# Optimization experiments

Measured on AMD Instinct MI355X. Metric: run time of the kernel, lower is better.

## Reference

```python
import jax, jax.numpy as jnp
import numpy as np

T, S, B, D, H, F, E = 1024, 1024, 4, 1024, 16, 4096, 8
HD = D // H
N = T * B                      # tokens entering MoE
CAP = 2 * N // E               # top-2 capacity per expert


def setup_inputs() -> dict:
    key = jax.random.key(0)
    ks = jax.random.split(key, 16)
    sc = 0.02
    rn = lambda k, shp, s=sc: jax.random.normal(k, shp, jnp.float32) * s
    return {
        "tgt": jax.random.normal(ks[0], (T, B, D), jnp.float32),
        "memory": jax.random.normal(ks[1], (S, B, D), jnp.float32),
        "sa_in_w": rn(ks[2], (3 * D, D)), "sa_in_b": jnp.zeros((3 * D,), jnp.float32),
        "sa_out_w": rn(ks[3], (D, D)), "sa_out_b": jnp.zeros((D,), jnp.float32),
        "ca_in_w": rn(ks[4], (3 * D, D)), "ca_in_b": jnp.zeros((3 * D,), jnp.float32),
        "ca_out_w": rn(ks[5], (D, D)), "ca_out_b": jnp.zeros((D,), jnp.float32),
        "ln1_g": jnp.ones((D,), jnp.float32), "ln1_b": jnp.zeros((D,), jnp.float32),
        "ln2_g": jnp.ones((D,), jnp.float32), "ln2_b": jnp.zeros((D,), jnp.float32),
        "ln3_g": jnp.ones((D,), jnp.float32), "ln3_b": jnp.zeros((D,), jnp.float32),
        "wg": rn(ks[6], (D, E)),
        "w1": rn(ks[7], (E, D, F)), "b1": jnp.zeros((E, F), jnp.float32),
        "w2": rn(ks[8], (E, F, D)), "b2": jnp.zeros((E, D), jnp.float32),
    }


def layer_norm(x, g, b, eps=1e-5):
    mu = jnp.mean(x, axis=-1, keepdims=True)
    var = jnp.var(x, axis=-1, keepdims=True)
    return (x - mu) * jax.lax.rsqrt(var + eps) * g + b


def mha(q_in, k_in, v_in, in_w, in_b, out_w, out_b):
    # q_in: [Tq,B,D], k_in/v_in: [Tk,B,D]; torch MultiheadAttention math (eval)
    wq, wk, wv = jnp.split(in_w, 3, axis=0)
    bq, bk, bv = jnp.split(in_b, 3)
    def heads(x, w, bias):
        y = x @ w.T + bias                       # [Tx,B,D]
        return y.reshape(x.shape[0], B, H, HD).transpose(1, 2, 0, 3)  # [B,H,Tx,hd]
    q, k, v = heads(q_in, wq, bq), heads(k_in, wk, bk), heads(v_in, wv, bv)
    scores = jnp.einsum('bhtd,bhsd->bhts', q, k) / np.sqrt(HD)
    attn = jax.nn.softmax(scores, axis=-1)
    o = jnp.einsum('bhts,bhsd->bhtd', attn, v)   # [B,H,Tq,hd]
    o = o.transpose(2, 0, 1, 3).reshape(q_in.shape[0], B, D)
    return o @ out_w.T + out_b


def moe_top2(x, wg, w1, b1, w2, b2):
    # x: [N,D]. Top-2 gating with capacity dispatch + grouped expert FFN.
    logits = x @ wg                               # [N,E]
    gates = jax.nn.softmax(logits, axis=-1)
    idx1 = jnp.argmax(gates, axis=-1)             # [N]
    m1 = jax.nn.one_hot(idx1, E, dtype=x.dtype)   # [N,E]
    gates_wo1 = jnp.where(m1 > 0, -jnp.inf, logits)
    idx2 = jnp.argmax(gates_wo1, axis=-1)
    m2 = jax.nn.one_hot(idx2, E, dtype=x.dtype)
    ar = jnp.arange(N)
    g1 = gates[ar, idx1]
    g2 = gates[ar, idx2]
    denom = g1 + g2 + 1e-9
    g1, g2 = g1 / denom, g2 / denom
    # positions within each expert buffer (first-come-first-serve, top1 before top2)
    pos1 = jnp.cumsum(m1, axis=0)[ar, idx1] - 1
    counts1 = jnp.sum(m1, axis=0)                 # [E]
    pos2 = jnp.cumsum(m2, axis=0)[ar, idx2] - 1 + counts1[idx2]
    keep1 = (pos1 < CAP).astype(x.dtype)
    keep2 = (pos2 < CAP).astype(x.dtype)
    p1 = jnp.clip(pos1, 0, CAP - 1).astype(jnp.int32)
    p2 = jnp.clip(pos2, 0, CAP - 1).astype(jnp.int32)
    buf = jnp.zeros((E, CAP, D), x.dtype)
    buf = buf.at[idx1, p1].add(x * keep1[:, None])
    buf = buf.at[idx2, p2].add(x * keep2[:, None])
    # grouped expert FFN: [E,CAP,D] -> [E,CAP,F] -> [E,CAP,D]
    h = jax.nn.relu(jnp.einsum('ecd,edf->ecf', buf, w1) + b1[:, None, :])
    eo = jnp.einsum('ecf,efd->ecd', h, w2) + b2[:, None, :]
    out = eo[idx1, p1] * (g1 * keep1)[:, None] + eo[idx2, p2] * (g2 * keep2)[:, None]
    return out


def reference(tgt, memory, sa_in_w, sa_in_b, sa_out_w, sa_out_b,
              ca_in_w, ca_in_b, ca_out_w, ca_out_b,
              ln1_g, ln1_b, ln2_g, ln2_b, ln3_g, ln3_b,
              wg, w1, b1, w2, b2):
    t2 = mha(tgt, tgt, tgt, sa_in_w, sa_in_b, sa_out_w, sa_out_b)
    x = layer_norm(tgt + t2, ln1_g, ln1_b)
    t2 = mha(x, memory, memory, ca_in_w, ca_in_b, ca_out_w, ca_out_b)
    x = layer_norm(x + t2, ln2_g, ln2_b)
    m = moe_top2(x.reshape(N, D), wg, w1, b1, w2, b2).reshape(T, B, D)
    x = layer_norm(x + m, ln3_g, ln3_b)
    return x
```

## Files before the change

kernel.cpp:

```cpp
#include <hip/hip_runtime.h>
#include <hip/hip_bf16.h>


typedef __bf16 bf16;
typedef __bf16 bf16x2 __attribute__((ext_vector_type(2)));
typedef __bf16 bf16x4 __attribute__((ext_vector_type(4)));
typedef __bf16 bf16x8 __attribute__((ext_vector_type(8)));
typedef float  f32x4  __attribute__((ext_vector_type(4)));

static_assert(sizeof(bf16) == 2, "bf16 size");

#define CAP_ 1024

#define GLOAD16(g, l)                                                  \
  __builtin_amdgcn_global_load_lds(                                    \
      (const __attribute__((address_space(1))) unsigned int*)(g),      \
      (__attribute__((address_space(3))) unsigned int*)(l), 16, 0, 0)

#define BAR() do { asm volatile("" ::: "memory"); __builtin_amdgcn_s_barrier(); asm volatile("" ::: "memory"); } while (0)

static const long OFF_WSAIN  = 0L;
static const long OFF_WSAOUT = 6291456L;
static const long OFF_WCAIN  = 8388608L;
static const long OFF_WCAOUT = 14680064L;
static const long OFF_BTGT   = 16777216L;
static const long OFF_BMEM   = 25165824L;
static const long OFF_QKV    = 33554432L;
static const long OFF_EO1    = 33554432L;
static const long OFF_KVCA   = OFF_QKV + 8388608L;
static const long OFF_VT     = 58720256L;
static const long OFF_AO     = 67108864L;
static const long OFF_PROJ   = 75497472L;
static const long OFF_X1     = 92274688L;
static const long OFF_X2     = 109051904L;
static const long OFF_SCORES = 125829120L;
static const long OFF_H      = OFF_SCORES + 67108864L;
static const long OFF_GATE   = 260046848L;
static const long OFF_E1   = OFF_GATE;
static const long OFF_E2   = OFF_GATE + 16384L;
static const long OFF_G1   = OFF_GATE + 32768L;
static const long OFF_G2   = OFF_GATE + 49152L;
static const long OFF_D1   = OFF_GATE + 65536L;
static const long OFF_D2   = OFF_GATE + 81920L;
static const long OFF_S1   = OFF_GATE + 98304L;
static const long OFF_S2   = OFF_GATE + 114688L;

__device__ __forceinline__ int xcd_swz(int bid, int nwg) {
  int q = nwg >> 3, r = nwg & 7;
  int xcd = bid & 7, idx = bid >> 3;
  return (xcd < r ? xcd * (q + 1) : r * (q + 1) + (xcd - r) * q) + idx;
}

__global__ __launch_bounds__(256) void k_cvt6(
    const float* __restrict__ s0, const float* __restrict__ s1,
    const float* __restrict__ s2, const float* __restrict__ s3,
    const float* __restrict__ s4, const float* __restrict__ s5,
    bf16* __restrict__ d0, bf16* __restrict__ d1, bf16* __restrict__ d2,
    bf16* __restrict__ d3, bf16* __restrict__ d4, bf16* __restrict__ d5) {
  long b = blockIdx.x;
  const float* s; bf16* d; long off;
  if (b < 3072)       { s = s0; d = d0; off = b; }
  else if (b < 4096)  { s = s1; d = d1; off = b - 3072; }
  else if (b < 7168)  { s = s2; d = d2; off = b - 4096; }
  else if (b < 8192)  { s = s3; d = d3; off = b - 7168; }
  else if (b < 12288) { s = s4; d = d4; off = b - 8192; }
  else                { s = s5; d = d5; off = b - 12288; }
  long i = off * 256 + threadIdx.x;
  float4 v = ((const float4*)s)[i];
  bf16x4 o = {(bf16)v.x, (bf16)v.y, (bf16)v.z, (bf16)v.w};
  ((bf16x4*)d)[i] = o;
}

__global__ __launch_bounds__(256) void k_transpose_f32_bf16(const float* __restrict__ in,
                                                            bf16* __restrict__ out, int R, int C) {
  __shared__ float t[64][70];
  int z = blockIdx.z;
  long r0 = (long)blockIdx.y * 64, c0 = (long)blockIdx.x * 64;
  const float* ib = in + (long)z * R * C;
  bf16* ob = out + (long)z * R * C;
  int x = threadIdx.x, y = threadIdx.y;
  #pragma unroll
  for (int j = 0; j < 4; j++) {
    int sr = y + j * 16;
    float4 v = *(const float4*)&ib[(r0 + sr) * C + c0 + x * 4];
    t[sr][x * 4 + 0] = v.x; t[sr][x * 4 + 1] = v.y;
    t[sr][x * 4 + 2] = v.z; t[sr][x * 4 + 3] = v.w;
  }
  __syncthreads();
  #pragma unroll
  for (int j = 0; j < 4; j++) {
    int sc = y + j * 16;
    #pragma unroll
    for (int i = 0; i < 2; i++) {
      int sr = x * 2 + i * 32;
      bf16x2 o = {(bf16)t[sr][sc], (bf16)t[sr + 1][sc]};
      *(bf16x2*)&ob[(c0 + sc) * R + r0 + sr] = o;
    }
  }
}

__global__ __launch_bounds__(256) void k_extract_vt(const bf16* __restrict__ in,
                                                    bf16* __restrict__ out, long rs, long sb) {
  __shared__ bf16 t[64][66];
  int z = blockIdx.z;
  long r0 = (long)blockIdx.y * 64;
  const bf16* ib = in + (long)(z >> 4) * sb + (long)(z & 15) * 64;
  bf16* ob = out + (long)z * 64 * 1024;
  int x = threadIdx.x, y = threadIdx.y;
  #pragma unroll
  for (int i = y; i < 64; i += 4) t[i][x] = ib[(r0 + i) * rs + x];
  __syncthreads();
  #pragma unroll
  for (int i = y; i < 64; i += 4) ob[(long)i * 1024 + r0 + x] = t[x][i];
}

template <int BM, int BN, int WM, int WN, bool RELU, typename OutT>
__global__ __launch_bounds__(256) void k_gemm_nt(
    const bf16* __restrict__ A, const bf16* __restrict__ Bp,
    OutT* __restrict__ C, const float* __restrict__ bias,
    int K, long lda, long ldb, long ldc, float alpha, int zdiv,
    long sA1, long sA0, long sB1, long sB0, long sC1, long sC0,
    long sBias1, long sBias0) {
  constexpr int BK = 32;
  constexpr int WTM = BM / WM, WTN = BN / WN, MR = WTM / 16, NR = WTN / 16;
  constexpr int AISS = BM * BK / 2048;
  constexpr int BISS = BN * BK / 2048;
  __shared__ bf16 sa[BM * BK];
  __shared__ bf16 sb[BN * BK];
  const int nwg = gridDim.x * gridDim.y * gridDim.z;
  const int bid = blockIdx.x + gridDim.x * (blockIdx.y + gridDim.y * blockIdx.z);
  const int lid = xcd_swz(bid, nwg);
  const int bx = lid % gridDim.x;
  const int rem = lid / gridDim.x;
  const int by = rem % gridDim.y;
  const int z = rem / gridDim.y;
  const int zh = z / zdiv, zl = z - zh * zdiv;
  const bf16* Ab = A + zh * sA1 + zl * sA0 + (long)by * BM * lda;
  const bf16* Bb = Bp + zh * sB1 + zl * sB0 + (long)bx * BN * ldb;
  const int tid = threadIdx.x, lane = tid & 63, wid = tid >> 6;
  const int wm = wid / WN, wn = wid % WN;

  const int srow = tid >> 2;
  const int scol = (tid & 3) * 8;
  const bf16* aptr[AISS];
  bf16* aldst[AISS];
  #pragma unroll
  for (int i = 0; i < AISS; i++) {
    aptr[i] = Ab + (long)(srow + i * 64) * lda + scol;
    aldst[i] = &sa[i * 2048 + (wid << 9)];
  }
  const bf16* bptr[BISS];
  bf16* bldst[BISS];
  #pragma unroll
  for (int i = 0; i < BISS; i++) {
    bptr[i] = Bb + (long)(srow + i * 64) * ldb + scol;
    bldst[i] = &sb[i * 2048 + (wid << 9)];
  }

  f32x4 acc[MR][NR] = {};
  const int rA = wm * WTM + (lane & 15);
  const int rB = wn * WTN + (lane & 15);
  const int kk = (lane >> 4) * 8;

  for (int k0 = 0; k0 < K; k0 += BK) {
    #pragma unroll
    for (int i = 0; i < AISS; i++) GLOAD16(aptr[i] + k0, aldst[i]);
    #pragma unroll
    for (int i = 0; i < BISS; i++) GLOAD16(bptr[i] + k0, bldst[i]);
    __syncthreads();
    bf16x8 af[MR], bfr[NR];
    #pragma unroll
    for (int mi = 0; mi < MR; mi++) af[mi] = *(const bf16x8*)&sa[(rA + mi * 16) * BK + kk];
    #pragma unroll
    for (int ni = 0; ni < NR; ni++) bfr[ni] = *(const bf16x8*)&sb[(rB + ni * 16) * BK + kk];
    #pragma unroll
    for (int mi = 0; mi < MR; mi++)
      #pragma unroll
      for (int ni = 0; ni < NR; ni++)
        acc[mi][ni] = __builtin_amdgcn_mfma_f32_16x16x32_bf16(af[mi], bfr[ni], acc[mi][ni], 0, 0, 0);
    __syncthreads();
  }
  OutT* Cb = C + zh * sC1 + zl * sC0;
  const float* biasb = bias ? (bias + zh * sBias1 + zl * sBias0) : nullptr;
  const long rowBase = (long)by * BM + wm * WTM + ((lane >> 4) * 4);
  const long colBase = (long)bx * BN + wn * WTN + (lane & 15);
  #pragma unroll
  for (int mi = 0; mi < MR; mi++) {
    #pragma unroll
    for (int ni = 0; ni < NR; ni++) {
      long col = colBase + ni * 16;
      float bv = biasb ? biasb[col] : 0.f;
      #pragma unroll
      for (int r = 0; r < 4; r++) {
        long row = rowBase + mi * 16 + r;
        float v = acc[mi][ni][r] * alpha + bv;
        if (RELU) v = fmaxf(v, 0.f);
        Cb[row * ldc + col] = (OutT)v;
      }
    }
  }
}

template <bool RELU, typename OutT>
__global__ __launch_bounds__(512, 2) void k_gemm8p(
    const bf16* __restrict__ A, const bf16* __restrict__ Bp,
    OutT* __restrict__ C, const float* __restrict__ bias,
    int K, long lda, long ldb, long ldc, int zdiv,
    long sA1, long sA0, long sB1, long sB0, long sC1, long sC0, long sBias1) {
  __shared__ bf16 smem[65536];
  const int nwg = gridDim.x * gridDim.y * gridDim.z;
  const int bid = blockIdx.x + gridDim.x * (blockIdx.y + gridDim.y * blockIdx.z);
  const int lid = xcd_swz(bid, nwg);
  const int bx = lid % gridDim.x;
  const int rem = lid / gridDim.x;
  const int by = rem % gridDim.y;
  const int z = rem / gridDim.y;
  const int zh = z / zdiv, zl = z - zh * zdiv;
  const bf16* Ab = A + zh * sA1 + zl * sA0 + (long)by * 256 * lda;
  const bf16* Bb = Bp + zh * sB1 + zl * sB0 + (long)bx * 256 * ldb;
  const int tid = threadIdx.x, lane = tid & 63, wid = tid >> 6;
  const int wm = wid >> 2, wn = wid & 3;
  const int lane15 = lane & 15, grp = lane >> 4;
  const int s_r = (wid << 3) + (lane >> 3);
  const int s_k = ((lane & 7) ^ (lane >> 3)) << 3;
  const int ldst = wid << 9;
  const int in0 = (grp << 4) ^ ((lane & 7) << 4);
  const int in1 = (64 | (grp << 4)) ^ ((lane & 7) << 4);

  const int NT = K >> 6;
  f32x4 acc[8][4] = {};
  bf16x8 a[4][2], b[2][2][2];

  const bf16* pA[4];
  const bf16* pB[4];
  #pragma unroll
  for (int q = 0; q < 4; q++) {
    pA[q] = Ab + (long)((q << 6) + s_r) * lda + s_k;
    pB[q] = Bb + (long)((q << 6) + s_r) * ldb + s_k;
  }

  auto loadA = [&](int mh, int cb) {
    #pragma unroll
    for (int mi2 = 0; mi2 < 4; mi2++) {
      int r = wm * 128 + mh * 64 + mi2 * 16 + lane15;
      a[mi2][0] = *(const bf16x8*)&smem[cb + (r << 6) + (in0 >> 1)];
      a[mi2][1] = *(const bf16x8*)&smem[cb + (r << 6) + (in1 >> 1)];
    }
  };
  auto loadB = [&](int nh, int cb) {
    #pragma unroll
    for (int ni2 = 0; ni2 < 2; ni2++) {
      int c = wn * 64 + nh * 32 + ni2 * 16 + lane15;
      b[nh][ni2][0] = *(const bf16x8*)&smem[cb + 16384 + (c << 6) + (in0 >> 1)];
      b[nh][ni2][1] = *(const bf16x8*)&smem[cb + 16384 + (c << 6) + (in1 >> 1)];
    }
  };
  auto mfmaQ = [&](int mh, int nh) {
    __builtin_amdgcn_s_setprio(1);
    #pragma unroll
    for (int ks = 0; ks < 2; ks++)
      #pragma unroll
      for (int mi2 = 0; mi2 < 4; mi2++)
        #pragma unroll
        for (int ni2 = 0; ni2 < 2; ni2++)
          acc[mh * 4 + mi2][nh * 2 + ni2] = __builtin_amdgcn_mfma_f32_16x16x32_bf16(
              a[mi2][ks], b[nh][ni2][ks], acc[mh * 4 + mi2][nh * 2 + ni2], 0, 0, 0);
    __builtin_amdgcn_s_setprio(0);
  };

  #pragma unroll
  for (int q = 0; q < 4; q++) {
    GLOAD16(pA[q], &smem[(q << 12) + ldst]);
    GLOAD16(pB[q], &smem[16384 + (q << 12) + ldst]);
  }
  #pragma unroll
  for (int q = 0; q < 4; q++) {
    GLOAD16(pA[q] + 64, &smem[32768 + (q << 12) + ldst]);
    GLOAD16(pB[q] + 64, &smem[32768 + 16384 + (q << 12) + ldst]);
  }
  asm volatile("s_waitcnt vmcnt(8)" ::: "memory");
  BAR();

  for (int t = 0; t < NT; t++) {
    const int cb = (t & 1) << 15;
    const bool dostage = (t + 2) < NT;
    loadA(0, cb); loadB(0, cb);
    BAR(); mfmaQ(0, 0); BAR();
    loadB(1, cb);
    if (dostage) {
      GLOAD16(pA[0] + 128, &smem[cb + ldst]);
      GLOAD16(pA[2] + 128, &smem[cb + (2 << 12) + ldst]);
    }
    BAR(); mfmaQ(0, 1); BAR();
    loadA(1, cb);
    if (dostage) {
      GLOAD16(pB[0] + 128, &smem[cb + 16384 + ldst]);
      GLOAD16(pB[1] + 128, &smem[cb + 16384 + (1 << 12) + ldst]);
    }
    BAR(); mfmaQ(1, 1); BAR();
    if (dostage) {
      GLOAD16(pA[1] + 128, &smem[cb + (1 << 12) + ldst]);
      GLOAD16(pA[3] + 128, &smem[cb + (3 << 12) + ldst]);
      GLOAD16(pB[2] + 128, &smem[cb + 16384 + (2 << 12) + ldst]);
      GLOAD16(pB[3] + 128, &smem[cb + 16384 + (3 << 12) + ldst]);
      asm volatile("s_waitcnt vmcnt(8)" ::: "memory");
    } else if (t + 1 < NT) {
      asm volatile("s_waitcnt vmcnt(0)" ::: "memory");
    }
    BAR(); mfmaQ(1, 0); BAR();
    #pragma unroll
    for (int q = 0; q < 4; q++) { pA[q] += 64; pB[q] += 64; }
  }

  OutT* Cb = C + zh * sC1 + zl * sC0;
  const float* biasb = bias ? (bias + zh * sBias1) : nullptr;
  float bv[4];
  #pragma unroll
  for (int ni = 0; ni < 4; ni++)
    bv[ni] = biasb ? biasb[(long)bx * 256 + wn * 64 + ni * 16 + lane15] : 0.f;
  const long rowBase = (long)by * 256 + wm * 128 + grp * 4;
  const long colBase = (long)bx * 256 + wn * 64 + lane15;
  #pragma unroll
  for (int mi = 0; mi < 8; mi++) {
    #pragma unroll
    for (int ni = 0; ni < 4; ni++) {
      long col = colBase + ni * 16;
      #pragma unroll
      for (int r = 0; r < 4; r++) {
        long row = rowBase + mi * 16 + r;
        float v = acc[mi][ni][r] + bv[ni];
        if (RELU) v = fmaxf(v, 0.f);
        Cb[row * ldc + col] = (OutT)v;
      }
    }
  }
}

__global__ __launch_bounds__(256) void k_flash(
    const bf16* __restrict__ q, const bf16* __restrict__ kk,
    const bf16* __restrict__ vt, bf16* __restrict__ ao,
    long qrs, long krs) {
  __shared__ bf16 kt[2][2048];
  __shared__ bf16 vtt[2][2048];
  __shared__ bf16 p_lds[4][32 * 72];
  const int nwg = gridDim.x * gridDim.y;
  const int bid = blockIdx.x + gridDim.x * blockIdx.y;
  const int lid = xcd_swz(bid, nwg);
  const int qt = lid & 7;
  const int bh = lid >> 3;
  const int b = bh >> 4, h = bh & 15;
  const int tid = threadIdx.x, lane = tid & 63, wid = tid >> 6;
  const int colLane = lane & 15, grp = lane >> 4;
  const bf16* qb = q + (qrs >> 2) * b + h * 64;
  const bf16* kb = kk + (krs >> 2) * b + h * 64;
  const bf16* vb = vt + (long)bh * 65536;

  bf16x8 qf[2][2];
  const int qrow0 = qt * 128 + wid * 32 + colLane;
  #pragma unroll
  for (int mi = 0; mi < 2; mi++)
    #pragma unroll
    for (int ks = 0; ks < 2; ks++)
      qf[mi][ks] = *(const bf16x8*)&qb[(long)(qrow0 + mi * 16) * qrs + ks * 32 + grp * 8];

  const int srow = tid >> 2;
  const int scol = (tid & 3) * 8;

  f32x4 oacc[2][4] = {};
  float m_[2][4], l_[2][4];
  #pragma unroll
  for (int mi = 0; mi < 2; mi++)
    #pragma unroll
    for (int r = 0; r < 4; r++) { m_[mi][r] = -INFINITY; l_[mi][r] = 0.f; }
  bf16* pl = &p_lds[wid][0];

  for (int s0 = 0; s0 < 1024; s0 += 64) {
    GLOAD16(&kb[(long)(s0 + srow) * krs + scol], &kt[0][wid << 9]);
    GLOAD16(&kb[(long)(s0 + srow) * krs + 32 + scol], &kt[1][wid << 9]);
    GLOAD16(&vb[(long)srow * 1024 + s0 + scol], &vtt[0][wid << 9]);
    GLOAD16(&vb[(long)srow * 1024 + s0 + 32 + scol], &vtt[1][wid << 9]);
    __syncthreads();

    f32x4 sacc[2][4] = {};
    bf16x8 kf[4][2];
    #pragma unroll
    for (int ni = 0; ni < 4; ni++)
      #pragma unroll
      for (int ks = 0; ks < 2; ks++)
        kf[ni][ks] = *(const bf16x8*)&kt[ks][(colLane + ni * 16) * 32 + grp * 8];
    #pragma unroll
    for (int ks = 0; ks < 2; ks++)
      #pragma unroll
      for (int mi = 0; mi < 2; mi++)
        #pragma unroll
        for (int ni = 0; ni < 4; ni++)
          sacc[mi][ni] = __builtin_amdgcn_mfma_f32_16x16x32_bf16(qf[mi][ks], kf[ni][ks], sacc[mi][ni], 0, 0, 0);

    float mnew[2][4], sc[2][4], psum[2][4];
    #pragma unroll
    for (int mi = 0; mi < 2; mi++)
      #pragma unroll
      for (int r = 0; r < 4; r++) {
        float vx = fmaxf(fmaxf(sacc[mi][0][r], sacc[mi][1][r]),
                         fmaxf(sacc[mi][2][r], sacc[mi][3][r])) * 0.125f;
        #pragma unroll
        for (int o = 1; o < 16; o <<= 1) vx = fmaxf(vx, __shfl_xor(vx, o));
        float mn = fmaxf(m_[mi][r], vx);
        sc[mi][r] = __expf(m_[mi][r] - mn);
        m_[mi][r] = mn; mnew[mi][r] = mn;
        l_[mi][r] *= sc[mi][r];
        psum[mi][r] = 0.f;
      }
    #pragma unroll
    for (int mi = 0; mi < 2; mi++)
      #pragma unroll
      for (int ni = 0; ni < 4; ni++)
        #pragma unroll
        for (int r = 0; r < 4; r++)
          oacc[mi][ni][r] *= sc[mi][r];
    #pragma unroll
    for (int mi = 0; mi < 2; mi++)
      #pragma unroll
      for (int ni = 0; ni < 4; ni++)
        #pragma unroll
        for (int r = 0; r < 4; r++) {
          float p = __expf(sacc[mi][ni][r] * 0.125f - mnew[mi][r]);
          psum[mi][r] += p;
          pl[(mi * 16 + grp * 4 + r) * 72 + ni * 16 + colLane] = (bf16)p;
        }
    #pragma unroll
    for (int mi = 0; mi < 2; mi++)
      #pragma unroll
      for (int r = 0; r < 4; r++) {
        float ps = psum[mi][r];
        #pragma unroll
        for (int o = 1; o < 16; o <<= 1) ps += __shfl_xor(ps, o);
        l_[mi][r] += ps;
      }

    bf16x8 pa[2][2], vf[4][2];
    #pragma unroll
    for (int mi = 0; mi < 2; mi++)
      #pragma unroll
      for (int ks = 0; ks < 2; ks++)
        pa[mi][ks] = *(const bf16x8*)&pl[(colLane + mi * 16) * 72 + ks * 32 + grp * 8];
    #pragma unroll
    for (int ni = 0; ni < 4; ni++)
      #pragma unroll
      for (int ks = 0; ks < 2; ks++)
        vf[ni][ks] = *(const bf16x8*)&vtt[ks][(colLane + ni * 16) * 32 + grp * 8];
    #pragma unroll
    for (int ks = 0; ks < 2; ks++)
      #pragma unroll
      for (int mi = 0; mi < 2; mi++)
        #pragma unroll
        for (int ni = 0; ni < 4; ni++)
          oacc[mi][ni] = __builtin_amdgcn_mfma_f32_16x16x32_bf16(pa[mi][ks], vf[ni][ks], oacc[mi][ni], 0, 0, 0);
    __syncthreads();
  }

  #pragma unroll
  for (int mi = 0; mi < 2; mi++)
    #pragma unroll
    for (int r = 0; r < 4; r++) {
      float inv = 1.f / l_[mi][r];
      int t = qt * 128 + wid * 32 + mi * 16 + grp * 4 + r;
      long n = (long)t * 4 + b;
      #pragma unroll
      for (int ni = 0; ni < 4; ni++)
        ao[n * 1024 + h * 64 + ni * 16 + colLane] = (bf16)(oacc[mi][ni][r] * inv);
    }
}

__global__ __launch_bounds__(256) void k_add_ln(const float* __restrict__ a, const float* __restrict__ b,
                                                const float* __restrict__ g, const float* __restrict__ be,
                                                float* __restrict__ out, bf16* __restrict__ outb) {
  long row = blockIdx.x;
  int tid = threadIdx.x;
  const float* pa = a + row * 1024;
  const float* pb = b + row * 1024;
  float v[4];
  float s = 0.f, sq = 0.f;
  #pragma unroll
  for (int i = 0; i < 4; i++) {
    int c = tid + i * 256;
    float x = pa[c] + pb[c];
    v[i] = x; s += x; sq += x * x;
  }
  #pragma unroll
  for (int o = 32; o; o >>= 1) { s += __shfl_xor(s, o); sq += __shfl_xor(sq, o); }
  __shared__ float r1[4], r2[4];
  int wid = tid >> 6;
  if ((tid & 63) == 0) { r1[wid] = s; r2[wid] = sq; }
  __syncthreads();
  s = r1[0] + r1[1] + r1[2] + r1[3];
  sq = r2[0] + r2[1] + r2[2] + r2[3];
  float mu = s * (1.f / 1024.f);
  float var = sq * (1.f / 1024.f) - mu * mu;
  float rstd = rsqrtf(var + 1e-5f);
  #pragma unroll
  for (int i = 0; i < 4; i++) {
    int c = tid + i * 256;
    float y = (v[i] - mu) * rstd * g[c] + be[c];
    out[row * 1024 + c] = y;
    if (outb) outb[row * 1024 + c] = (bf16)y;
  }
}

__global__ __launch_bounds__(256) void k_gate(const float* __restrict__ x, const float* __restrict__ wg,
                                              int* __restrict__ e1, int* __restrict__ e2,
                                              float* __restrict__ g1, float* __restrict__ g2) {
  int n = blockIdx.x * 4 + (threadIdx.x >> 6);
  int lane = threadIdx.x & 63;
  const float* xr = x + (long)n * 1024;
  float acc[8] = {0.f, 0.f, 0.f, 0.f, 0.f, 0.f, 0.f, 0.f};
  for (int i = 0; i < 16; i++) {
    float xv = xr[i * 64 + lane];
    const float* wr = wg + (long)(i * 64 + lane) * 8;
    #pragma unroll
    for (int e = 0; e < 8; e++) acc[e] += xv * wr[e];
  }
  #pragma unroll
  for (int e = 0; e < 8; e++)
    #pragma unroll
    for (int o = 32; o; o >>= 1) acc[e] += __shfl_xor(acc[e], o);
  if (lane == 0) {
    int i1 = 0; float b1v = acc[0];
    #pragma unroll
    for (int e = 1; e < 8; e++) if (acc[e] > b1v) { b1v = acc[e]; i1 = e; }
    int i2 = -1; float b2v = -INFINITY;
    #pragma unroll
    for (int e = 0; e < 8; e++) if (e != i1 && acc[e] > b2v) { b2v = acc[e]; i2 = e; }
    float den = 0.f;
    #pragma unroll
    for (int e = 0; e < 8; e++) den += __expf(acc[e] - b1v);
    float gg1 = 1.f / den;
    float gg2 = __expf(b2v - b1v) / den;
    float dn = gg1 + gg2 + 1e-9f;
    e1[n] = i1; e2[n] = i2; g1[n] = gg1 / dn; g2[n] = gg2 / dn;
  }
}

__global__ __launch_bounds__(256) void k_positions(const int* __restrict__ e1, const int* __restrict__ e2,
                                                   const float* __restrict__ g1, const float* __restrict__ g2,
                                                   int* __restrict__ d1, int* __restrict__ d2,
                                                   float* __restrict__ s1, float* __restrict__ s2) {
  const int e = blockIdx.x;
  const int tid = threadIdx.x, lane = tid & 63, wid = tid >> 6;
  __shared__ int wsum[4];
  int f[16];
  int cnt = 0;
  #pragma unroll
  for (int i = 0; i < 16; i++) { f[i] = (e1[tid * 16 + i] == e) ? 1 : 0; cnt += f[i]; }
  int inc = cnt;
  #pragma unroll
  for (int o = 1; o < 64; o <<= 1) { int v = __shfl_up(inc, o); if (lane >= o) inc += v; }
  if (lane == 63) wsum[wid] = inc;
  __syncthreads();
  int base = inc - cnt;
  for (int w = 0; w < wid; w++) base += wsum[w];
  const int total1 = wsum[0] + wsum[1] + wsum[2] + wsum[3];
  int run = base;
  #pragma unroll
  for (int i = 0; i < 16; i++) {
    int n = tid * 16 + i;
    if (f[i]) {
      int p = run++;
      d1[n] = e * CAP_ + (p < CAP_ ? p : CAP_ - 1);
      s1[n] = (p < CAP_) ? g1[n] : 0.f;
    }
  }
  cnt = 0;
  #pragma unroll
  for (int i = 0; i < 16; i++) { f[i] = (e2[tid * 16 + i] == e) ? 1 : 0; cnt += f[i]; }
  inc = cnt;
  #pragma unroll
  for (int o = 1; o < 64; o <<= 1) { int v = __shfl_up(inc, o); if (lane >= o) inc += v; }
  __syncthreads();
  if (lane == 63) wsum[wid] = inc;
  __syncthreads();
  base = inc - cnt + total1;
  for (int w = 0; w < wid; w++) base += wsum[w];
  run = base;
  #pragma unroll
  for (int i = 0; i < 16; i++) {
    int n = tid * 16 + i;
    if (f[i]) {
      int p = run++;
      d2[n] = e * CAP_ + (p < CAP_ ? p : CAP_ - 1);
      s2[n] = (p < CAP_) ? g2[n] : 0.f;
    }
  }
}

__global__ __launch_bounds__(256) void k_scatter(const float* __restrict__ x, const int* __restrict__ d1,
                                                 const int* __restrict__ d2, const float* __restrict__ s1,
                                                 const float* __restrict__ s2, bf16* __restrict__ buf) {
  int n = blockIdx.x;
  int tid = threadIdx.x;
  const float* xr = x + (long)n * 1024;
  float v[4];
  #pragma unroll
  for (int i = 0; i < 4; i++) v[i] = xr[tid + i * 256];
  if (s1[n] != 0.f) {
    bf16* o = buf + (long)d1[n] * 1024;
    #pragma unroll
    for (int i = 0; i < 4; i++) o[tid + i * 256] = (bf16)v[i];
  }
  if (s2[n] != 0.f) {
    bf16* o = buf + (long)d2[n] * 1024;
    #pragma unroll
    for (int i = 0; i < 4; i++) o[tid + i * 256] = (bf16)v[i];
  }
}

__global__ __launch_bounds__(256) void k_gather_ln(const float* __restrict__ x,
                                                   const bf16* __restrict__ p0, const bf16* __restrict__ p1,
                                                   const float* __restrict__ b2,
                                                   const int* __restrict__ d1, const int* __restrict__ d2,
                                                   const float* __restrict__ s1, const float* __restrict__ s2,
                                                   const float* __restrict__ g, const float* __restrict__ be,
                                                   float* __restrict__ out) {
  long n = blockIdx.x;
  int tid = threadIdx.x;
  float a1 = s1[n], a2 = s2[n];
  long i1 = (long)d1[n] * 1024, i2 = (long)d2[n] * 1024;
  long e1b = (long)(d1[n] >> 10) * 1024, e2b = (long)(d2[n] >> 10) * 1024;
  const float* xr = x + n * 1024;
  float v[4];
  float s = 0.f, sq = 0.f;
  #pragma unroll
  for (int i = 0; i < 4; i++) {
    int c = tid + i * 256;
    float r1v = (float)p0[i1 + c] + (float)p1[i1 + c] + b2[e1b + c];
    float r2v = (float)p0[i2 + c] + (float)p1[i2 + c] + b2[e2b + c];
    float y = xr[c] + a1 * r1v + a2 * r2v;
    v[i] = y; s += y; sq += y * y;
  }
  #pragma unroll
  for (int o = 32; o; o >>= 1) { s += __shfl_xor(s, o); sq += __shfl_xor(sq, o); }
  __shared__ float r1[4], r2[4];
  int wid = tid >> 6;
  if ((tid & 63) == 0) { r1[wid] = s; r2[wid] = sq; }
  __syncthreads();
  s = r1[0] + r1[1] + r1[2] + r1[3];
  sq = r2[0] + r2[1] + r2[2] + r2[3];
  float mu = s * (1.f / 1024.f);
  float var = sq * (1.f / 1024.f) - mu * mu;
  float rstd = rsqrtf(var + 1e-5f);
  #pragma unroll
  for (int i = 0; i < 4; i++) {
    int c = tid + i * 256;
    out[n * 1024 + c] = (v[i] - mu) * rstd * g[c] + be[c];
  }
}

extern "C" void kernel_launch(void* const* d_in, const int* in_sizes, int n_in,
                              void* d_out, int out_size, void* d_ws, size_t ws_size,
                              hipStream_t stream) {
  const float* tgt      = (const float*)d_in[0];
  const float* memory   = (const float*)d_in[1];
  const float* sa_in_w  = (const float*)d_in[2];
  const float* sa_in_b  = (const float*)d_in[3];
  const float* sa_out_w = (const float*)d_in[4];
  const float* sa_out_b = (const float*)d_in[5];
  const float* ca_in_w  = (const float*)d_in[6];
  const float* ca_in_b  = (const float*)d_in[7];
  const float* ca_out_w = (const float*)d_in[8];
  const float* ca_out_b = (const float*)d_in[9];
  const float* ln1_g    = (const float*)d_in[10];
  const float* ln1_b    = (const float*)d_in[11];
  const float* ln2_g    = (const float*)d_in[12];
  const float* ln2_b    = (const float*)d_in[13];
  const float* ln3_g    = (const float*)d_in[14];
  const float* ln3_b    = (const float*)d_in[15];
  const float* wg       = (const float*)d_in[16];
  const float* w1       = (const float*)d_in[17];
  const float* b1       = (const float*)d_in[18];
  const float* w2       = (const float*)d_in[19];
  const float* b2       = (const float*)d_in[20];

  char* ws = (char*)d_ws;
  auto B16 = [&](long o) { return (bf16*)(ws + o); };
  auto F32 = [&](long o) { return (float*)(ws + o); };
  auto I32 = [&](long o) { return (int*)(ws + o); };

  const dim3 blk256(256), blk512(512), blkT16(16, 16), blkT(64, 4);

  k_cvt6<<<16384, blk256, 0, stream>>>(sa_in_w, sa_out_w, ca_in_w, ca_out_w, tgt, memory,
                                       B16(OFF_WSAIN), B16(OFF_WSAOUT), B16(OFF_WCAIN),
                                       B16(OFF_WCAOUT), B16(OFF_BTGT), B16(OFF_BMEM));

  k_gemm8p<false, bf16><<<dim3(12, 16, 1), blk512, 0, stream>>>(
      B16(OFF_BTGT), B16(OFF_WSAIN), B16(OFF_QKV), sa_in_b,
      1024, 1024, 1024, 3072, 1, 0, 0, 0, 0, 0, 0, 0);
  k_extract_vt<<<dim3(1, 16, 64), blkT, 0, stream>>>(B16(OFF_QKV) + 2048, B16(OFF_VT), 12288, 3072);
  k_flash<<<dim3(8, 64), blk256, 0, stream>>>(
      B16(OFF_QKV), B16(OFF_QKV) + 1024, B16(OFF_VT), B16(OFF_AO), 12288, 12288);
  k_gemm_nt<128, 64, 4, 1, false, float><<<dim3(16, 32, 1), blk256, 0, stream>>>(
      B16(OFF_AO), B16(OFF_WSAOUT), F32(OFF_PROJ), sa_out_b,
      1024, 1024, 1024, 1024, 1.f, 1, 0, 0, 0, 0, 0, 0, 0, 0);
  k_add_ln<<<4096, blk256, 0, stream>>>(tgt, F32(OFF_PROJ), ln1_g, ln1_b, F32(OFF_X1), B16(OFF_BTGT));

  k_gemm_nt<128, 64, 4, 1, false, bf16><<<dim3(16, 32, 1), blk256, 0, stream>>>(
      B16(OFF_BTGT), B16(OFF_WCAIN), B16(OFF_QKV), ca_in_b,
      1024, 1024, 1024, 1024, 1.f, 1, 0, 0, 0, 0, 0, 0, 0, 0);
  k_gemm_nt<128, 64, 4, 1, false, bf16><<<dim3(32, 32, 1), blk256, 0, stream>>>(
      B16(OFF_BMEM), B16(OFF_WCAIN) + 1024L * 1024, B16(OFF_KVCA), ca_in_b + 1024,
      1024, 1024, 1024, 2048, 1.f, 1, 0, 0, 0, 0, 0, 0, 0, 0);
  k_extract_vt<<<dim3(1, 16, 64), blkT, 0, stream>>>(B16(OFF_KVCA) + 1024, B16(OFF_VT), 8192, 2048);
  k_flash<<<dim3(8, 64), blk256, 0, stream>>>(
      B16(OFF_QKV), B16(OFF_KVCA), B16(OFF_VT), B16(OFF_AO), 4096, 8192);
  k_gemm_nt<128, 64, 4, 1, false, float><<<dim3(16, 32, 1), blk256, 0, stream>>>(
      B16(OFF_AO), B16(OFF_WCAOUT), F32(OFF_PROJ), ca_out_b,
      1024, 1024, 1024, 1024, 1.f, 1, 0, 0, 0, 0, 0, 0, 0, 0);
  k_add_ln<<<4096, blk256, 0, stream>>>(F32(OFF_X1), F32(OFF_PROJ), ln2_g, ln2_b, F32(OFF_X2), (bf16*)nullptr);

  k_gate<<<1024, blk256, 0, stream>>>(F32(OFF_X2), wg, I32(OFF_E1), I32(OFF_E2), F32(OFF_G1), F32(OFF_G2));
  k_positions<<<8, blk256, 0, stream>>>(I32(OFF_E1), I32(OFF_E2), F32(OFF_G1), F32(OFF_G2),
                                        I32(OFF_D1), I32(OFF_D2), F32(OFF_S1), F32(OFF_S2));
  k_scatter<<<4096, blk256, 0, stream>>>(F32(OFF_X2), I32(OFF_D1), I32(OFF_D2),
                                         F32(OFF_S1), F32(OFF_S2), B16(OFF_QKV));
  k_transpose_f32_bf16<<<dim3(64, 16, 8), blkT16, 0, stream>>>(w1, B16(OFF_SCORES), 1024, 4096);
  k_gemm8p<true, bf16><<<dim3(16, 4, 8), blk512, 0, stream>>>(
      B16(OFF_QKV), B16(OFF_SCORES), B16(OFF_H), b1,
      1024, 1024, 1024, 4096, 1,
      1048576, 0, 4194304, 0, 4194304, 0, 4096);
  k_transpose_f32_bf16<<<dim3(16, 64, 8), blkT16, 0, stream>>>(w2, B16(OFF_SCORES), 4096, 1024);
  k_gemm8p<false, bf16><<<dim3(4, 4, 16), blk512, 0, stream>>>(
      B16(OFF_H), B16(OFF_SCORES), B16(OFF_PROJ), nullptr,
      2048, 4096, 4096, 1024, 2,
      4194304, 2048, 4194304, 2048, 1048576, (OFF_EO1 - OFF_PROJ) / 2, 0);
  k_gather_ln<<<4096, blk256, 0, stream>>>(F32(OFF_X2), B16(OFF_PROJ), B16(OFF_EO1), b2,
                                           I32(OFF_D1), I32(OFF_D2),
                                           F32(OFF_S1), F32(OFF_S2), ln3_g, ln3_b, (float*)d_out);

  (void)in_sizes; (void)n_in; (void)out_size; (void)ws_size;
}
```

Baseline: 557.7 us.

## Batch-major Q/K/V layout, reschedule gemm8p LDS reads, vectorize elementwise kernels

QKV projections now write separate batch-major Q, K and V buffers through a row permutation in the GEMM epilogue. Flash attention and V-transpose therefore read contiguous rows with a fixed stride. The gemm8p main loop reorders its LDS fragment loads and global staging so the next tile's B fragment is prefetched before the last MFMA quarter. The transpose, layernorm, gate, scatter and gather kernels are vectorized to float4/bf16x8 accesses. This adds strided permuted stores in GEMM epilogues and a changed barrier schedule that must stay correct.

```diff
diff --git a/kernel.cpp b/kernel.cpp
--- a/kernel.cpp
+++ b/kernel.cpp
@@ -26,8 +26,10 @@
 static const long OFF_BTGT   = 16777216L;
 static const long OFF_BMEM   = 25165824L;
 static const long OFF_QKV    = 33554432L;
+static const long OFF_QS     = OFF_QKV;
+static const long OFF_KS     = OFF_QKV + 8388608L;
+static const long OFF_VS     = OFF_QKV + 16777216L;
 static const long OFF_EO1    = 33554432L;
-static const long OFF_KVCA   = OFF_QKV + 8388608L;
 static const long OFF_VT     = 58720256L;
 static const long OFF_AO     = 67108864L;
 static const long OFF_PROJ   = 75497472L;
@@ -73,12 +75,13 @@
 
 __global__ __launch_bounds__(256) void k_transpose_f32_bf16(const float* __restrict__ in,
                                                             bf16* __restrict__ out, int R, int C) {
-  __shared__ float t[64][70];
+  __shared__ float t[64][66];
   int z = blockIdx.z;
   long r0 = (long)blockIdx.y * 64, c0 = (long)blockIdx.x * 64;
   const float* ib = in + (long)z * R * C;
   bf16* ob = out + (long)z * R * C;
-  int x = threadIdx.x, y = threadIdx.y;
+  int tid = threadIdx.x;
+  int x = tid & 15, y = tid >> 4;
   #pragma unroll
   for (int j = 0; j < 4; j++) {
     int sr = y + j * 16;
@@ -87,34 +90,43 @@
     t[sr][x * 4 + 2] = v.z; t[sr][x * 4 + 3] = v.w;
   }
   __syncthreads();
+  int xs = tid & 7, jj = tid >> 3;
+  #pragma unroll
+  for (int p = 0; p < 2; p++) {
+    int c = jj + p * 32;
+    bf16x8 o;
+    #pragma unroll
+    for (int k = 0; k < 8; k++) o[k] = (bf16)t[xs * 8 + k][c];
+    *(bf16x8*)&ob[(c0 + c) * R + r0 + xs * 8] = o;
+  }
+}
+
+__global__ __launch_bounds__(256) void k_extract_vt(const bf16* __restrict__ in,
+                                                    bf16* __restrict__ out) {
+  __shared__ bf16 t[64][68];
+  const int bh = blockIdx.y;
+  const long r0 = (long)blockIdx.x * 64;
+  const bf16* ib = in + (long)bh * 65536 + ((long)(bh >> 4) * 983040);
+  const int b = bh >> 4, h = bh & 15;
+  ib = in + (long)b * 1048576 + h * 64;
+  bf16* ob = out + (long)bh * 65536;
+  int tid = threadIdx.x;
+  int x = tid & 15, y = tid >> 4;
   #pragma unroll
   for (int j = 0; j < 4; j++) {
-    int sc = y + j * 16;
-    #pragma unroll
-    for (int i = 0; i < 2; i++) {
-      int sr = x * 2 + i * 32;
-      bf16x2 o = {(bf16)t[sr][sc], (bf16)t[sr + 1][sc]};
-      *(bf16x2*)&ob[(c0 + sc) * R + r0 + sr] = o;
-    }
-  }
-}
-
-__global__ __launch_bounds__(256) void k_extract_vt(const bf16* __restrict__ in,
-                                                    bf16* __restrict__ out, long rs, long sb) {
-  __shared__ bf16 t[64][66];
-  int z = blockIdx.z;
-  long r0 = (long)blockIdx.y * 64;
-  const bf16* ib = in + (long)(z >> 4) * sb + (long)(z & 15) * 64;
-  bf16* ob = out + (long)z * 64 * 1024;
-  int x = threadIdx.x, y = threadIdx.y;
-  #pragma unroll
-  for (int i = y; i < 64; i += 4) t[i][x] = ib[(r0 + i) * rs + x];
+    int sr = y + j * 16;
+    *(bf16x4*)&t[sr][x * 4] = *(const bf16x4*)&ib[(r0 + sr) * 1024 + x * 4];
+  }
   __syncthreads();
   #pragma unroll
-  for (int i = y; i < 64; i += 4) ob[(long)i * 1024 + r0 + x] = t[x][i];
-}
-
-template <int BM, int BN, int WM, int WN, bool RELU, typename OutT>
+  for (int p = 0; p < 4; p++) {
+    int c = y + p * 16;
+    bf16x4 o = {t[x * 4 + 0][c], t[x * 4 + 1][c], t[x * 4 + 2][c], t[x * 4 + 3][c]};
+    *(bf16x4*)&ob[(long)c * 1024 + r0 + x * 4] = o;
+  }
+}
+
+template <int BM, int BN, int WM, int WN, bool RELU, bool PERM, typename OutT>
 __global__ __launch_bounds__(256) void k_gemm_nt(
     const bf16* __restrict__ A, const bf16* __restrict__ Bp,
     OutT* __restrict__ C, const float* __restrict__ bias,
@@ -193,15 +205,16 @@
       #pragma unroll
       for (int r = 0; r < 4; r++) {
         long row = rowBase + mi * 16 + r;
+        long prow = PERM ? ((row & 3) * 1024 + (row >> 2)) : row;
         float v = acc[mi][ni][r] * alpha + bv;
         if (RELU) v = fmaxf(v, 0.f);
-        Cb[row * ldc + col] = (OutT)v;
+        Cb[prow * ldc + col] = (OutT)v;
       }
     }
   }
 }
 
-template <bool RELU, typename OutT>
+template <bool RELU, bool PERM, typename OutT>
 __global__ __launch_bounds__(512, 2) void k_gemm8p(
     const bf16* __restrict__ A, const bf16* __restrict__ Bp,
     OutT* __restrict__ C, const float* __restrict__ bias,
@@ -280,34 +293,45 @@
   }
   asm volatile("s_waitcnt vmcnt(8)" ::: "memory");
   BAR();
+  loadB(0, 0);
 
   for (int t = 0; t < NT; t++) {
     const int cb = (t & 1) << 15;
     const bool dostage = (t + 2) < NT;
-    loadA(0, cb); loadB(0, cb);
-    BAR(); mfmaQ(0, 0); BAR();
+    const bool doread = (t + 1) < NT;
+    loadA(0, cb);
+    BAR();
     loadB(1, cb);
+    mfmaQ(0, 0);
+    BAR();
     if (dostage) {
       GLOAD16(pA[0] + 128, &smem[cb + ldst]);
       GLOAD16(pA[2] + 128, &smem[cb + (2 << 12) + ldst]);
     }
-    BAR(); mfmaQ(0, 1); BAR();
+    BAR();
+    mfmaQ(0, 1);
+    BAR();
     loadA(1, cb);
     if (dostage) {
       GLOAD16(pB[0] + 128, &smem[cb + 16384 + ldst]);
       GLOAD16(pB[1] + 128, &smem[cb + 16384 + (1 << 12) + ldst]);
-    }
-    BAR(); mfmaQ(1, 1); BAR();
+      GLOAD16(pB[2] + 128, &smem[cb + 16384 + (2 << 12) + ldst]);
+      GLOAD16(pB[3] + 128, &smem[cb + 16384 + (3 << 12) + ldst]);
+    }
+    BAR();
+    mfmaQ(1, 0);
+    BAR();
     if (dostage) {
       GLOAD16(pA[1] + 128, &smem[cb + (1 << 12) + ldst]);
       GLOAD16(pA[3] + 128, &smem[cb + (3 << 12) + ldst]);
-      GLOAD16(pB[2] + 128, &smem[cb + 16384 + (2 << 12) + ldst]);
-      GLOAD16(pB[3] + 128, &smem[cb + 16384 + (3 << 12) + ldst]);
       asm volatile("s_waitcnt vmcnt(8)" ::: "memory");
-    } else if (t + 1 < NT) {
+    } else if (doread) {
       asm volatile("s_waitcnt vmcnt(0)" ::: "memory");
     }
-    BAR(); mfmaQ(1, 0); BAR();
+    BAR();
+    if (doread) loadB(0, cb ^ 32768);
+    mfmaQ(1, 1);
+    BAR();
     #pragma unroll
     for (int q = 0; q < 4; q++) { pA[q] += 64; pB[q] += 64; }
   }
@@ -328,9 +352,10 @@
       #pragma unroll
       for (int r = 0; r < 4; r++) {
         long row = rowBase + mi * 16 + r;
+        long prow = PERM ? ((row & 3) * 1024 + (row >> 2)) : row;
         float v = acc[mi][ni][r] + bv[ni];
         if (RELU) v = fmaxf(v, 0.f);
-        Cb[row * ldc + col] = (OutT)v;
+        Cb[prow * ldc + col] = (OutT)v;
       }
     }
   }
@@ -338,8 +363,7 @@
 
 __global__ __launch_bounds__(256) void k_flash(
     const bf16* __restrict__ q, const bf16* __restrict__ kk,
-    const bf16* __restrict__ vt, bf16* __restrict__ ao,
-    long qrs, long krs) {
+    const bf16* __restrict__ vt, bf16* __restrict__ ao) {
   __shared__ bf16 kt[2][2048];
   __shared__ bf16 vtt[2][2048];
   __shared__ bf16 p_lds[4][32 * 72];
@@ -351,8 +375,8 @@
   const int b = bh >> 4, h = bh & 15;
   const int tid = threadIdx.x, lane = tid & 63, wid = tid >> 6;
   const int colLane = lane & 15, grp = lane >> 4;
-  const bf16* qb = q + (qrs >> 2) * b + h * 64;
-  const bf16* kb = kk + (krs >> 2) * b + h * 64;
+  const bf16* qb = q + (long)b * 1048576 + h * 64;
+  const bf16* kb = kk + (long)b * 1048576 + h * 64;
   const bf16* vb = vt + (long)bh * 65536;
 
   bf16x8 qf[2][2];
@@ -361,7 +385,7 @@
   for (int mi = 0; mi < 2; mi++)
     #pragma unroll
     for (int ks = 0; ks < 2; ks++)
-      qf[mi][ks] = *(const bf16x8*)&qb[(long)(qrow0 + mi * 16) * qrs + ks * 32 + grp * 8];
+      qf[mi][ks] = *(const bf16x8*)&qb[(long)(qrow0 + mi * 16) * 1024 + ks * 32 + grp * 8];
 
   const int srow = tid >> 2;
   const int scol = (tid & 3) * 8;
@@ -375,8 +399,8 @@
   bf16* pl = &p_lds[wid][0];
 
   for (int s0 = 0; s0 < 1024; s0 += 64) {
-    GLOAD16(&kb[(long)(s0 + srow) * krs + scol], &kt[0][wid << 9]);
-    GLOAD16(&kb[(long)(s0 + srow) * krs + 32 + scol], &kt[1][wid << 9]);
+    GLOAD16(&kb[(long)(s0 + srow) * 1024 + scol], &kt[0][wid << 9]);
+    GLOAD16(&kb[(long)(s0 + srow) * 1024 + 32 + scol], &kt[1][wid << 9]);
     GLOAD16(&vb[(long)srow * 1024 + s0 + scol], &vtt[0][wid << 9]);
     GLOAD16(&vb[(long)srow * 1024 + s0 + 32 + scol], &vtt[1][wid << 9]);
     __syncthreads();
@@ -477,16 +501,11 @@
                                                 float* __restrict__ out, bf16* __restrict__ outb) {
   long row = blockIdx.x;
   int tid = threadIdx.x;
-  const float* pa = a + row * 1024;
-  const float* pb = b + row * 1024;
-  float v[4];
-  float s = 0.f, sq = 0.f;
-  #pragma unroll
-  for (int i = 0; i < 4; i++) {
-    int c = tid + i * 256;
-    float x = pa[c] + pb[c];
-    v[i] = x; s += x; sq += x * x;
-  }
+  float4 va = ((const float4*)(a + row * 1024))[tid];
+  float4 vb = ((const float4*)(b + row * 1024))[tid];
+  float v[4] = {va.x + vb.x, va.y + vb.y, va.z + vb.z, va.w + vb.w};
+  float s = v[0] + v[1] + v[2] + v[3];
+  float sq = v[0] * v[0] + v[1] * v[1] + v[2] * v[2] + v[3] * v[3];
   #pragma unroll
   for (int o = 32; o; o >>= 1) { s += __shfl_xor(s, o); sq += __shfl_xor(sq, o); }
   __shared__ float r1[4], r2[4];
@@ -498,12 +517,16 @@
   float mu = s * (1.f / 1024.f);
   float var = sq * (1.f / 1024.f) - mu * mu;
   float rstd = rsqrtf(var + 1e-5f);
-  #pragma unroll
-  for (int i = 0; i < 4; i++) {
-    int c = tid + i * 256;
-    float y = (v[i] - mu) * rstd * g[c] + be[c];
-    out[row * 1024 + c] = y;
-    if (outb) outb[row * 1024 + c] = (bf16)y;
+  float4 vg = ((const float4*)g)[tid];
+  float4 vbe = ((const float4*)be)[tid];
+  float y0 = (v[0] - mu) * rstd * vg.x + vbe.x;
+  float y1 = (v[1] - mu) * rstd * vg.y + vbe.y;
+  float y2 = (v[2] - mu) * rstd * vg.z + vbe.z;
+  float y3 = (v[3] - mu) * rstd * vg.w + vbe.w;
+  ((float4*)(out + row * 1024))[tid] = make_float4(y0, y1, y2, y3);
+  if (outb) {
+    bf16x4 o = {(bf16)y0, (bf16)y1, (bf16)y2, (bf16)y3};
+    ((bf16x4*)(outb + row * 1024))[tid] = o;
   }
 }
 
@@ -517,8 +540,10 @@
   for (int i = 0; i < 16; i++) {
     float xv = xr[i * 64 + lane];
     const float* wr = wg + (long)(i * 64 + lane) * 8;
-    #pragma unroll
-    for (int e = 0; e < 8; e++) acc[e] += xv * wr[e];
+    float4 w0 = *(const float4*)wr;
+    float4 w1v = *(const float4*)(wr + 4);
+    acc[0] += xv * w0.x; acc[1] += xv * w0.y; acc[2] += xv * w0.z; acc[3] += xv * w0.w;
+    acc[4] += xv * w1v.x; acc[5] += xv * w1v.y; acc[6] += xv * w1v.z; acc[7] += xv * w1v.w;
   }
   #pragma unroll
   for (int e = 0; e < 8; e++)
@@ -598,20 +623,10 @@
                                                  const float* __restrict__ s2, bf16* __restrict__ buf) {
   int n = blockIdx.x;
   int tid = threadIdx.x;
-  const float* xr = x + (long)n * 1024;
-  float v[4];
-  #pragma unroll
-  for (int i = 0; i < 4; i++) v[i] = xr[tid + i * 256];
-  if (s1[n] != 0.f) {
-    bf16* o = buf + (long)d1[n] * 1024;
-    #pragma unroll
-    for (int i = 0; i < 4; i++) o[tid + i * 256] = (bf16)v[i];
-  }
-  if (s2[n] != 0.f) {
-    bf16* o = buf + (long)d2[n] * 1024;
-    #pragma unroll
-    for (int i = 0; i < 4; i++) o[tid + i * 256] = (bf16)v[i];
-  }
+  float4 v = ((const float4*)(x + (long)n * 1024))[tid];
+  bf16x4 o = {(bf16)v.x, (bf16)v.y, (bf16)v.z, (bf16)v.w};
+  if (s1[n] != 0.f) ((bf16x4*)(buf + (long)d1[n] * 1024))[tid] = o;
+  if (s2[n] != 0.f) ((bf16x4*)(buf + (long)d2[n] * 1024))[tid] = o;
 }
 
 __global__ __launch_bounds__(256) void k_gather_ln(const float* __restrict__ x,
@@ -626,15 +641,23 @@
   float a1 = s1[n], a2 = s2[n];
   long i1 = (long)d1[n] * 1024, i2 = (long)d2[n] * 1024;
   long e1b = (long)(d1[n] >> 10) * 1024, e2b = (long)(d2[n] >> 10) * 1024;
-  const float* xr = x + n * 1024;
+  float4 vx = ((const float4*)(x + n * 1024))[tid];
+  bf16x4 q10 = *(const bf16x4*)&p0[i1 + tid * 4];
+  bf16x4 q11 = *(const bf16x4*)&p1[i1 + tid * 4];
+  bf16x4 q20 = *(const bf16x4*)&p0[i2 + tid * 4];
+  bf16x4 q21 = *(const bf16x4*)&p1[i2 + tid * 4];
+  float4 vb1 = ((const float4*)(b2 + e1b))[tid];
+  float4 vb2 = ((const float4*)(b2 + e2b))[tid];
   float v[4];
+  float xs[4] = {vx.x, vx.y, vx.z, vx.w};
+  float b1a[4] = {vb1.x, vb1.y, vb1.z, vb1.w};
+  float b2a[4] = {vb2.x, vb2.y, vb2.z, vb2.w};
   float s = 0.f, sq = 0.f;
   #pragma unroll
   for (int i = 0; i < 4; i++) {
-    int c = tid + i * 256;
-    float r1v = (float)p0[i1 + c] + (float)p1[i1 + c] + b2[e1b + c];
-    float r2v = (float)p0[i2 + c] + (float)p1[i2 + c] + b2[e2b + c];
-    float y = xr[c] + a1 * r1v + a2 * r2v;
+    float r1v = (float)q10[i] + (float)q11[i] + b1a[i];
+    float r2v = (float)q20[i] + (float)q21[i] + b2a[i];
+    float y = xs[i] + a1 * r1v + a2 * r2v;
     v[i] = y; s += y; sq += y * y;
   }
   #pragma unroll
@@ -648,11 +671,16 @@
   float mu = s * (1.f / 1024.f);
   float var = sq * (1.f / 1024.f) - mu * mu;
   float rstd = rsqrtf(var + 1e-5f);
-  #pragma unroll
-  for (int i = 0; i < 4; i++) {
-    int c = tid + i * 256;
-    out[n * 1024 + c] = (v[i] - mu) * rstd * g[c] + be[c];
-  }
+  float4 vg = ((const float4*)g)[tid];
+  float4 vbe = ((const float4*)be)[tid];
+  float ga[4] = {vg.x, vg.y, vg.z, vg.w};
+  float ba[4] = {vbe.x, vbe.y, vbe.z, vbe.w};
+  float4 o;
+  o.x = (v[0] - mu) * rstd * ga[0] + ba[0];
+  o.y = (v[1] - mu) * rstd * ga[1] + ba[1];
+  o.z = (v[2] - mu) * rstd * ga[2] + ba[2];
+  o.w = (v[3] - mu) * rstd * ga[3] + ba[3];
+  ((float4*)(out + n * 1024))[tid] = o;
 }
 
 extern "C" void kernel_launch(void* const* d_in, const int* in_sizes, int n_in,
@@ -685,33 +713,33 @@
   auto F32 = [&](long o) { return (float*)(ws + o); };
   auto I32 = [&](long o) { return (int*)(ws + o); };
 
-  const dim3 blk256(256), blk512(512), blkT16(16, 16), blkT(64, 4);
+  const dim3 blk256(256), blk512(512);
 
   k_cvt6<<<16384, blk256, 0, stream>>>(sa_in_w, sa_out_w, ca_in_w, ca_out_w, tgt, memory,
                                        B16(OFF_WSAIN), B16(OFF_WSAOUT), B16(OFF_WCAIN),
                                        B16(OFF_WCAOUT), B16(OFF_BTGT), B16(OFF_BMEM));
 
-  k_gemm8p<false, bf16><<<dim3(12, 16, 1), blk512, 0, stream>>>(
-      B16(OFF_BTGT), B16(OFF_WSAIN), B16(OFF_QKV), sa_in_b,
-      1024, 1024, 1024, 3072, 1, 0, 0, 0, 0, 0, 0, 0);
-  k_extract_vt<<<dim3(1, 16, 64), blkT, 0, stream>>>(B16(OFF_QKV) + 2048, B16(OFF_VT), 12288, 3072);
-  k_flash<<<dim3(8, 64), blk256, 0, stream>>>(
-      B16(OFF_QKV), B16(OFF_QKV) + 1024, B16(OFF_VT), B16(OFF_AO), 12288, 12288);
-  k_gemm_nt<128, 64, 4, 1, false, float><<<dim3(16, 32, 1), blk256, 0, stream>>>(
+  k_gemm8p<false, true, bf16><<<dim3(4, 16, 3), blk512, 0, stream>>>(
+      B16(OFF_BTGT), B16(OFF_WSAIN), B16(OFF_QS), sa_in_b,
+      1024, 1024, 1024, 1024, 1,
+      0, 0, 1048576, 0, 4194304, 0, 1024);
+  k_extract_vt<<<dim3(16, 64), blk256, 0, stream>>>(B16(OFF_VS), B16(OFF_VT));
+  k_flash<<<dim3(8, 64), blk256, 0, stream>>>(B16(OFF_QS), B16(OFF_KS), B16(OFF_VT), B16(OFF_AO));
+  k_gemm_nt<128, 64, 4, 1, false, false, float><<<dim3(16, 32, 1), blk256, 0, stream>>>(
       B16(OFF_AO), B16(OFF_WSAOUT), F32(OFF_PROJ), sa_out_b,
       1024, 1024, 1024, 1024, 1.f, 1, 0, 0, 0, 0, 0, 0, 0, 0);
   k_add_ln<<<4096, blk256, 0, stream>>>(tgt, F32(OFF_PROJ), ln1_g, ln1_b, F32(OFF_X1), B16(OFF_BTGT));
 
-  k_gemm_nt<128, 64, 4, 1, false, bf16><<<dim3(16, 32, 1), blk256, 0, stream>>>(
-      B16(OFF_BTGT), B16(OFF_WCAIN), B16(OFF_QKV), ca_in_b,
+  k_gemm_nt<128, 64, 4, 1, false, true, bf16><<<dim3(16, 32, 1), blk256, 0, stream>>>(
+      B16(OFF_BTGT), B16(OFF_WCAIN), B16(OFF_QS), ca_in_b,
       1024, 1024, 1024, 1024, 1.f, 1, 0, 0, 0, 0, 0, 0, 0, 0);
-  k_gemm_nt<128, 64, 4, 1, false, bf16><<<dim3(32, 32, 1), blk256, 0, stream>>>(
-      B16(OFF_BMEM), B16(OFF_WCAIN) + 1024L * 1024, B16(OFF_KVCA), ca_in_b + 1024,
-      1024, 1024, 1024, 2048, 1.f, 1, 0, 0, 0, 0, 0, 0, 0, 0);
-  k_extract_vt<<<dim3(1, 16, 64), blkT, 0, stream>>>(B16(OFF_KVCA) + 1024, B16(OFF_VT), 8192, 2048);
-  k_flash<<<dim3(8, 64), blk256, 0, stream>>>(
-      B16(OFF_QKV), B16(OFF_KVCA), B16(OFF_VT), B16(OFF_AO), 4096, 8192);
-  k_gemm_nt<128, 64, 4, 1, false, float><<<dim3(16, 32, 1), blk256, 0, stream>>>(
+  k_gemm_nt<128, 64, 4, 1, false, true, bf16><<<dim3(16, 32, 2), blk256, 0, stream>>>(
+      B16(OFF_BMEM), B16(OFF_WCAIN) + 1024L * 1024, B16(OFF_KS), ca_in_b + 1024,
+      1024, 1024, 1024, 1024, 1.f, 1,
+      0, 0, 1048576, 0, 4194304, 0, 1024, 0);
+  k_extract_vt<<<dim3(16, 64), blk256, 0, stream>>>(B16(OFF_VS), B16(OFF_VT));
+  k_flash<<<dim3(8, 64), blk256, 0, stream>>>(B16(OFF_QS), B16(OFF_KS), B16(OFF_VT), B16(OFF_AO));
+  k_gemm_nt<128, 64, 4, 1, false, false, float><<<dim3(16, 32, 1), blk256, 0, stream>>>(
       B16(OFF_AO), B16(OFF_WCAOUT), F32(OFF_PROJ), ca_out_b,
       1024, 1024, 1024, 1024, 1.f, 1, 0, 0, 0, 0, 0, 0, 0, 0);
   k_add_ln<<<4096, blk256, 0, stream>>>(F32(OFF_X1), F32(OFF_PROJ), ln2_g, ln2_b, F32(OFF_X2), (bf16*)nullptr);
@@ -721,13 +749,13 @@
                                         I32(OFF_D1), I32(OFF_D2), F32(OFF_S1), F32(OFF_S2));
   k_scatter<<<4096, blk256, 0, stream>>>(F32(OFF_X2), I32(OFF_D1), I32(OFF_D2),
                                          F32(OFF_S1), F32(OFF_S2), B16(OFF_QKV));
-  k_transpose_f32_bf16<<<dim3(64, 16, 8), blkT16, 0, stream>>>(w1, B16(OFF_SCORES), 1024, 4096);
-  k_gemm8p<true, bf16><<<dim3(16, 4, 8), blk512, 0, stream>>>(
+  k_transpose_f32_bf16<<<dim3(64, 16, 8), blk256, 0, stream>>>(w1, B16(OFF_SCORES), 1024, 4096);
+  k_gemm8p<true, false, bf16><<<dim3(16, 4, 8), blk512, 0, stream>>>(
       B16(OFF_QKV), B16(OFF_SCORES), B16(OFF_H), b1,
       1024, 1024, 1024, 4096, 1,
       1048576, 0, 4194304, 0, 4194304, 0, 4096);
-  k_transpose_f32_bf16<<<dim3(16, 64, 8), blkT16, 0, stream>>>(w2, B16(OFF_SCORES), 4096, 1024);
-  k_gemm8p<false, bf16><<<dim3(4, 4, 16), blk512, 0, stream>>>(
+  k_transpose_f32_bf16<<<dim3(16, 64, 8), blk256, 0, stream>>>(w2, B16(OFF_SCORES), 4096, 1024);
+  k_gemm8p<false, false, bf16><<<dim3(4, 4, 16), blk512, 0, stream>>>(
       B16(OFF_H), B16(OFF_SCORES), B16(OFF_PROJ), nullptr,
       2048, 4096, 4096, 1024, 2,
       4194304, 2048, 4194304, 2048, 1048576, (OFF_EO1 - OFF_PROJ) / 2, 0);
```

New measurement: 550.8 us. About the same (-1.2%).
